# Optimization experiments

Measured on AMD Instinct MI355X. Metric: run time of the kernel, lower is better.

## Reference

```python
import jax, jax.numpy as jnp
import numpy as np

D_HEAD = 64
IGNORE = -100000.0


def setup_inputs() -> dict:
    key = jax.random.key(0)
    ks = jax.random.split(key, 5)
    B, S, D, H, M = 2, 2048, 768, 12, D_HEAD
    scale = 0.05  # 'random_normal' keras init stddev
    return {
        "x": jax.random.normal(ks[0], (B, S, D), jnp.float32),
        "W_Q": jax.random.normal(ks[1], (H, D, M), jnp.float32) * scale,
        "b_Q": jnp.zeros((H, M), jnp.float32),
        "W_K": jax.random.normal(ks[2], (H, D, M), jnp.float32) * scale,
        "b_K": jnp.zeros((H, M), jnp.float32),
        "W_V": jax.random.normal(ks[3], (H, D, M), jnp.float32) * scale,
        "b_V": jnp.zeros((H, M), jnp.float32),
        "W_O": jax.random.normal(ks[4], (H, M, D), jnp.float32) * scale,
        "b_O": jnp.zeros((D,), jnp.float32),
    }


def reference(x, W_Q, b_Q, W_K, b_K, W_V, b_V, W_O, b_O):
    # q,k,v: [b, s, h, m]
    q = jnp.einsum("bqd,hdm->bqhm", x, W_Q) + b_Q
    k = jnp.einsum("bkd,hdm->bkhm", x, W_K) + b_K
    v = jnp.einsum("bkd,hdm->bkhm", x, W_V) + b_V
    # scores: [b, h, q, k], scaled by 1/sqrt(d_head)
    scores = jnp.einsum("bqhm,bkhm->bhqk", q, k) / jnp.sqrt(
        jnp.asarray(D_HEAD, q.dtype)
    )
    S = x.shape[1]
    # causal mask: strictly-upper-triangular positions set to IGNORE (-1e5),
    # matching tf.where(mask == 1, IGNORE, scores)
    causal = jnp.arange(S)[:, None] >= jnp.arange(S)[None, :]  # [q, k]
    scores = jnp.where(causal[None, None, :, :], scores, jnp.asarray(IGNORE, scores.dtype))
    pattern = jax.nn.softmax(scores, axis=-1)
    z = jnp.einsum("bhqk,bkhm->bqhm", pattern, v)
    attn_out = jnp.einsum("bqhm,hmd->bqd", z, W_O) + b_O
    return attn_out
```

## Files before the change

### kernel.cpp

```cpp
#include <hip/hip_runtime.h>
#include <hip/hip_bf16.h>
#include <cstdint>
#include <cstddef>

#define B_ 2
#define S_ 2048
#define D_ 768
#define H_ 12
#define M_ 64
#define BS_ (B_ * S_)
#define NQKV_ 2304
#define NCHUNK_ 80
#define TOTCHUNK_ (24 * NCHUNK_)
#define QSCALE 0.18033688011f

typedef __attribute__((ext_vector_type(8))) short bf16x8;
typedef __attribute__((ext_vector_type(4))) short bf16x4;
typedef __attribute__((ext_vector_type(4))) float f32x4;

__device__ __forceinline__ unsigned short f2bu(float f) {
    __hip_bfloat16 h = __float2bfloat16(f);
    unsigned short u;
    __builtin_memcpy(&u, &h, 2);
    return u;
}
__device__ __forceinline__ unsigned pack2(float a, float b) {
    return (unsigned)f2bu(a) | ((unsigned)f2bu(b) << 16);
}

__device__ __forceinline__ bf16x8 ld16(const unsigned short* p) {
    p = (const unsigned short*)__builtin_assume_aligned(p, 16);
    bf16x8 v; __builtin_memcpy(&v, p, 16); return v;
}
__device__ __forceinline__ bf16x4 ld8(const unsigned short* p) {
    p = (const unsigned short*)__builtin_assume_aligned(p, 8);
    bf16x4 v; __builtin_memcpy(&v, p, 8); return v;
}
__device__ __forceinline__ uint4 ld16u(const unsigned short* p) {
    p = (const unsigned short*)__builtin_assume_aligned(p, 16);
    uint4 v; __builtin_memcpy(&v, p, 16); return v;
}
__device__ __forceinline__ void st16(unsigned short* p, uint4 v) {
    p = (unsigned short*)__builtin_assume_aligned(p, 16);
    __builtin_memcpy(p, &v, 16);
}
__device__ __forceinline__ void st8(unsigned short* p, uint2 v) {
    p = (unsigned short*)__builtin_assume_aligned(p, 8);
    __builtin_memcpy(p, &v, 8);
}
__device__ __forceinline__ float4 ldf4(const float* p) {
    p = (const float*)__builtin_assume_aligned(p, 16);
    float4 v; __builtin_memcpy(&v, p, 16); return v;
}
__device__ __forceinline__ void async16(const unsigned short* g, unsigned short* l) {
    __builtin_amdgcn_global_load_lds(
        (const __attribute__((address_space(1))) void*)g,
        (__attribute__((address_space(3))) void*)l, 16, 0, 0);
}
__device__ __forceinline__ void b82f(uint4 u, float* o) {
    o[0] = __uint_as_float(u.x << 16); o[1] = __uint_as_float(u.x & 0xffff0000u);
    o[2] = __uint_as_float(u.y << 16); o[3] = __uint_as_float(u.y & 0xffff0000u);
    o[4] = __uint_as_float(u.z << 16); o[5] = __uint_as_float(u.z & 0xffff0000u);
    o[6] = __uint_as_float(u.w << 16); o[7] = __uint_as_float(u.w & 0xffff0000u);
}

#define NEG_BIG (-3.0e38f)

__global__ void prep(const float* __restrict__ WQ, const float* __restrict__ WK,
                     const float* __restrict__ WV, const float* __restrict__ WO,
                     const float* __restrict__ x,
                     unsigned short* __restrict__ WT,
                     unsigned short* __restrict__ WOT,
                     unsigned short* __restrict__ xb)
{
    const int bx = blockIdx.x;
    if (bx < 216) {
        const int xx = bx % 9, yy = bx / 9;
        const int c  = xx * 256 + threadIdx.x;
        const int k0 = yy * 32;
        const int which = c / D_;
        const int r = c - which * D_;
        const int h = r >> 6, m = r & 63;
        const float* Wsel = (which == 0) ? WQ : (which == 1) ? WK : WV;
        const float* src = Wsel + (size_t)h * D_ * M_ + m;
        unsigned short* dst = WT + (size_t)c * D_ + k0;
        for (int i = 0; i < 32; i += 8) {
            float wv[8];
#pragma unroll
            for (int j = 0; j < 8; j++) wv[j] = src[(size_t)(k0 + i + j) * M_];
            uint4 pu;
            pu.x = pack2(wv[0], wv[1]); pu.y = pack2(wv[2], wv[3]);
            pu.z = pack2(wv[4], wv[5]); pu.w = pack2(wv[6], wv[7]);
            st16(dst + i, pu);
        }
    } else if (bx < 288) {
        const int b2 = bx - 216;
        const int xx = b2 % 3, yy = b2 / 3;
        const int c  = xx * 256 + threadIdx.x;
        const int k0 = yy * 32;
        unsigned short* dst = WOT + (size_t)c * D_ + k0;
        for (int i = 0; i < 32; i += 8) {
            float wv[8];
#pragma unroll
            for (int j = 0; j < 8; j++) wv[j] = WO[(size_t)(k0 + i + j) * D_ + c];
            uint4 pu;
            pu.x = pack2(wv[0], wv[1]); pu.y = pack2(wv[2], wv[3]);
            pu.z = pack2(wv[4], wv[5]); pu.w = pack2(wv[6], wv[7]);
            st16(dst + i, pu);
        }
    } else {
        const size_t i = ((size_t)(bx - 288) * 256 + threadIdx.x) * 16;
#pragma unroll
        for (int p = 0; p < 2; p++) {
            float4 a0 = ldf4(x + i + p * 8), a1 = ldf4(x + i + p * 8 + 4);
            uint4 u;
            u.x = pack2(a0.x, a0.y); u.y = pack2(a0.z, a0.w);
            u.z = pack2(a1.x, a1.y); u.w = pack2(a1.z, a1.w);
            st16(xb + i + p * 8, u);
        }
    }
}

__global__ __launch_bounds__(256, 2) void qkv_gemm(
    const unsigned short* __restrict__ xb,
    const unsigned short* __restrict__ WT,
    const float* __restrict__ bQ, const float* __restrict__ bK,
    const float* __restrict__ bV,
    unsigned short* __restrict__ qo, unsigned short* __restrict__ ko,
    unsigned short* __restrict__ vt)
{
    const int row0 = blockIdx.x * 128;
    const int col0 = blockIdx.y * 96;
    const int t = threadIdx.x;
    const int w = t >> 6, lane = t & 63, quad = lane >> 4, l16 = lane & 15;
    const int wrow0 = (w & 1) * 64, wcol0 = (w >> 1) * 48;

    __shared__ unsigned short Alds[128 * 64];
    __shared__ unsigned short Blds[96 * 64];

    f32x4 acc[4][3] = {};

    const unsigned short* asrc[4];
    const unsigned short* bsrc[3];
    int ldsoffA[4], ldsoffB[3];
#pragma unroll
    for (int q = 0; q < 4; q++) {
        const int cq = w * 256 + q * 64 + lane;
        const int row = cq >> 3, c = cq & 7;
        const int cs = c ^ (row & 7);
        asrc[q] = xb + (size_t)(row0 + row) * D_ + cs * 8;
        ldsoffA[q] = (w * 256 + q * 64) * 8;
    }
#pragma unroll
    for (int q = 0; q < 3; q++) {
        const int cq = w * 192 + q * 64 + lane;
        const int row = cq >> 3, c = cq & 7;
        const int cs = c ^ (row & 7);
        bsrc[q] = WT + (size_t)(col0 + row) * D_ + cs * 8;
        ldsoffB[q] = (w * 192 + q * 64) * 8;
    }
    const int swz = (l16 & 7);

    for (int k0 = 0; k0 < D_; k0 += 64) {
#pragma unroll
        for (int q = 0; q < 4; q++) async16(asrc[q] + k0, Alds + ldsoffA[q]);
#pragma unroll
        for (int q = 0; q < 3; q++) async16(bsrc[q] + k0, Blds + ldsoffB[q]);
        __syncthreads();

        bf16x8 af[4][2], bfm[3][2];
#pragma unroll
        for (int rt = 0; rt < 4; rt++) {
            const int row = wrow0 + rt * 16 + l16;
#pragma unroll
            for (int hh = 0; hh < 2; hh++)
                af[rt][hh] = ld16(&Alds[row * 64 + ((hh * 4 + quad) ^ swz) * 8]);
        }
#pragma unroll
        for (int st = 0; st < 3; st++) {
            const int row = wcol0 + st * 16 + l16;
#pragma unroll
            for (int hh = 0; hh < 2; hh++)
                bfm[st][hh] = ld16(&Blds[row * 64 + ((hh * 4 + quad) ^ swz) * 8]);
        }
#pragma unroll
        for (int rt = 0; rt < 4; rt++)
#pragma unroll
            for (int st = 0; st < 3; st++) {
                acc[rt][st] = __builtin_amdgcn_mfma_f32_16x16x32_bf16(
                    af[rt][0], bfm[st][0], acc[rt][st], 0, 0, 0);
                acc[rt][st] = __builtin_amdgcn_mfma_f32_16x16x32_bf16(
                    af[rt][1], bfm[st][1], acc[rt][st], 0, 0, 0);
            }
        __syncthreads();
    }

    const int which = col0 / D_;
    const int colin = col0 - which * D_;

    if (which == 0) {
#pragma unroll
        for (int st = 0; st < 3; st++) {
            const int cl = colin + wcol0 + st * 16 + l16;
            const int h = cl >> 6, m = cl & 63;
            const float bval = bQ[cl];
#pragma unroll
            for (int rt = 0; rt < 4; rt++)
#pragma unroll
                for (int rr = 0; rr < 4; rr++) {
                    const int R = row0 + wrow0 + rt * 16 + quad * 4 + rr;
                    const int bb = R >> 11, s = R & (S_ - 1);
                    qo[(((size_t)bb * H_ + h) * S_ + s) * M_ + m] =
                        f2bu((acc[rt][st][rr] + bval) * QSCALE);
                }
        }
    } else if (which == 1) {
#pragma unroll
        for (int st = 0; st < 3; st++) {
            const int cl = colin + wcol0 + st * 16 + l16;
            const int h = cl >> 6, m = cl & 63;
            const int blk = m >> 3, inn = m & 7;
            const float bval = bK[cl];
#pragma unroll
            for (int rt = 0; rt < 4; rt++)
#pragma unroll
                for (int rr = 0; rr < 4; rr++) {
                    const int R = row0 + wrow0 + rt * 16 + quad * 4 + rr;
                    const int bb = R >> 11, s = R & (S_ - 1);
                    ko[(((size_t)bb * H_ + h) * S_ + s) * M_ +
                       ((blk ^ (s & 7)) << 3) + inn] =
                        f2bu(acc[rt][st][rr] + bval);
                }
        }
    } else {
#pragma unroll
        for (int st = 0; st < 3; st++) {
            const int cl = colin + wcol0 + st * 16 + l16;
            const int h = cl >> 6, m = cl & 63;
            const float bval = bV[cl];
#pragma unroll
            for (int rt = 0; rt < 4; rt++) {
                const int R0 = row0 + wrow0 + rt * 16 + quad * 4;
                const int bb = R0 >> 11, s0 = R0 & (S_ - 1);
                const int tile = s0 >> 7;
                const int gl = (s0 & 127) >> 2;
                const int pl = gl >> 1, hi = gl & 1;
                const int pp = pl ^ ((m >> 1) & 7);
                const int half = hi ^ (m & 1);
                uint2 v;
                v.x = pack2(acc[rt][st][0] + bval, acc[rt][st][1] + bval);
                v.y = pack2(acc[rt][st][2] + bval, acc[rt][st][3] + bval);
                st8(&vt[(((size_t)bb * H_ + h) * 16 + tile) * (M_ * 128)
                        + m * 128 + (pp * 2 + half) * 4], v);
            }
        }
    }
}

__global__ __launch_bounds__(256, 2) void attn_split(
    const unsigned short* __restrict__ Q,
    const unsigned short* __restrict__ Kin,
    const unsigned short* __restrict__ Vt,
    unsigned short* __restrict__ Opart,
    float* __restrict__ ml,
    unsigned short* __restrict__ Z)
{
    const int flat = blockIdx.y * NCHUNK_ + blockIdx.x;
    const int bh = flat % 24;
    const int xx = (NCHUNK_ - 1) - flat / 24;

    int qt, c, nc;
    if (xx < 8)       { qt = xx; c = 0; nc = 1; }
    else if (xx < 24) { int u = xx - 8;  qt = 8  + (u >> 1); c = u & 1;  nc = 2; }
    else if (xx < 48) { int u = xx - 24; qt = 16 + u / 3;    c = u % 3;  nc = 3; }
    else              { int u = xx - 48; qt = 24 + (u >> 2); c = u & 3;  nc = 4; }

    const int ci     = bh * NCHUNK_ + xx;
    const int kbeg   = c * 512;
    const int keyend = min((qt + 1) * 64, kbeg + 512);
    const int iters  = (keyend - kbeg + 127) >> 7;
    const bool lastchunk = (c == nc - 1);

    const int t = threadIdx.x;
    const int wave = t >> 6, lane = t & 63, quad = lane >> 4, l16 = lane & 15;

    const unsigned short* Qb  = Q   + ((size_t)bh * S_ + qt * 64) * M_;
    const unsigned short* Kb  = Kin + (size_t)bh * S_ * M_;
    const unsigned short* Vb  = Vt  + (size_t)bh * M_ * S_;

    __shared__ unsigned short Klds[128 * 64];
    __shared__ unsigned short Vlds[64 * 128];

    bf16x8 qf[2];
    {
        const unsigned short* qrow = Qb + (size_t)(wave * 16 + l16) * M_;
        qf[0] = ld16(qrow + quad * 8);
        qf[1] = ld16(qrow + 32 + quad * 8);
    }

    const int ksw = l16 & 7;
    const int ko0 = (quad ^ ksw) * 8;
    const int ko1 = ((quad + 4) ^ ksw) * 8;
    int voff[8];
#pragma unroll
    for (int st = 0; st < 8; st++)
        voff[st] = l16 * 128 + (quad ^ (l16 & 3)) * 4
                 + ((st ^ ((l16 >> 2) & 3)) << 4);

    const int wdst = wave * 64 * 8;

    f32x4 o_acc[4] = {};
    float lrow = 0.f;

    for (int it = 0; it < iters; it++) {
        __syncthreads();
        const int key0 = kbeg + it * 128;
        const unsigned short* kt = Kb + (size_t)key0 * M_;
        const unsigned short* vtile = Vb + (size_t)(key0 >> 7) * (M_ * 128);
#pragma unroll
        for (int q = 0; q < 4; q++)
            async16(kt + (size_t)(q * 256 + t) * 8, Klds + q * 2048 + wdst);
#pragma unroll
        for (int q = 0; q < 4; q++)
            async16(vtile + (size_t)(q * 256 + t) * 8, Vlds + q * 2048 + wdst);
        __syncthreads();

        f32x4 s_acc[8];
#pragma unroll
        for (int st = 0; st < 8; st++) {
            f32x4 z4 = {0.f, 0.f, 0.f, 0.f};
            const unsigned short* krow = &Klds[(st * 16 + l16) * 64];
            bf16x8 k0 = ld16(krow + ko0);
            bf16x8 k1 = ld16(krow + ko1);
            z4 = __builtin_amdgcn_mfma_f32_16x16x32_bf16(k0, qf[0], z4, 0, 0, 0);
            z4 = __builtin_amdgcn_mfma_f32_16x16x32_bf16(k1, qf[1], z4, 0, 0, 0);
            s_acc[st] = z4;
        }

        if (lastchunk && it == iters - 1) {
            const int keyq = kbeg + it * 128 + quad * 4;
            const int qg = qt * 64 + wave * 16 + l16;
#pragma unroll
            for (int st = 0; st < 8; st++)
#pragma unroll
                for (int r = 0; r < 4; r++)
                    if (keyq + st * 16 + r > qg)
                        s_acc[st][r] = -1e30f;
        }

        bf16x4 pkv[8];
#pragma unroll
        for (int st = 0; st < 8; st++) {
            float p0 = exp2f(s_acc[st][0]);
            float p1 = exp2f(s_acc[st][1]);
            float p2 = exp2f(s_acc[st][2]);
            float p3 = exp2f(s_acc[st][3]);
            lrow += (p0 + p1) + (p2 + p3);
            uint2 u;
            u.x = pack2(p0, p1);
            u.y = pack2(p2, p3);
            __builtin_memcpy(&pkv[st], &u, 8);
        }

#pragma unroll
        for (int stf = 0; stf < 4; stf++) {
#pragma unroll
            for (int st = 0; st < 8; st++) {
                bf16x4 va = ld8(&Vlds[stf * 2048 + voff[st]]);
                o_acc[stf] = __builtin_amdgcn_mfma_f32_16x16x16bf16_1k(
                    va, pkv[st], o_acc[stf], 0, 0, 0);
            }
        }
    }

    lrow += __shfl_xor(lrow, 16, 64);
    lrow += __shfl_xor(lrow, 32, 64);

    const int q = wave * 16 + l16;
    if (nc == 1) {
        const float invL = 1.0f / lrow;
        const int b = bh / H_, h = bh - b * H_;
        unsigned short* zp =
            Z + ((size_t)b * S_ + qt * 64 + q) * (H_ * M_) + h * M_;
#pragma unroll
        for (int stf = 0; stf < 4; stf++) {
            uint2 u;
            u.x = pack2(o_acc[stf][0] * invL, o_acc[stf][1] * invL);
            u.y = pack2(o_acc[stf][2] * invL, o_acc[stf][3] * invL);
            st8(&zp[stf * 16 + quad * 4], u);
        }
    } else {
        unsigned short* Op = Opart + (size_t)ci * 4096;
#pragma unroll
        for (int stf = 0; stf < 4; stf++) {
            uint2 u;
            u.x = pack2(o_acc[stf][0], o_acc[stf][1]);
            u.y = pack2(o_acc[stf][2], o_acc[stf][3]);
            st8(&Op[q * 64 + stf * 16 + quad * 4], u);
        }
        if (quad == 0)
            ml[(size_t)ci * 128 + 64 + q] = lrow;
    }
}

__global__ void combine(const unsigned short* __restrict__ Opart,
                        const float* __restrict__ ml,
                        unsigned short* __restrict__ Z)
{
    const int qt = blockIdx.x + 8, bh = blockIdx.y;
    const int b = bh / H_, h = bh - b * H_;
    const int g = qt >> 3, r7 = qt & 7;
    const int nc = g + 1;
    const int base = bh * NCHUNK_ + qt + 4 * g * (g - 1) + r7 * g;

    const int t = threadIdx.x;
    const int q = t >> 2, fs = (t & 3) * 16;

    float L = 0.f;
    for (int c = 0; c < nc; c++)
        L += ml[(size_t)(base + c) * 128 + 64 + q];
    const float invL = 1.0f / L;

    float o[16] = {};
    for (int c = 0; c < nc; c++) {
        const unsigned short* op =
            Opart + (size_t)(base + c) * 4096 + q * 64 + fs;
        float f[8];
        b82f(ld16u(op), f);
#pragma unroll
        for (int j = 0; j < 8; j++) o[j] += f[j];
        b82f(ld16u(op + 8), f);
#pragma unroll
        for (int j = 0; j < 8; j++) o[8 + j] += f[j];
    }

    unsigned short* zp =
        Z + ((size_t)b * S_ + qt * 64 + q) * (H_ * M_) + h * M_ + fs;
    uint4 u0, u1;
    u0.x = pack2(o[0]*invL,  o[1]*invL);  u0.y = pack2(o[2]*invL,  o[3]*invL);
    u0.z = pack2(o[4]*invL,  o[5]*invL);  u0.w = pack2(o[6]*invL,  o[7]*invL);
    u1.x = pack2(o[8]*invL,  o[9]*invL);  u1.y = pack2(o[10]*invL, o[11]*invL);
    u1.z = pack2(o[12]*invL, o[13]*invL); u1.w = pack2(o[14]*invL, o[15]*invL);
    st16(zp, u0);
    st16(zp + 8, u1);
}

__global__ __launch_bounds__(256, 2) void oproj_gemm(
    const unsigned short* __restrict__ Zin,
    const unsigned short* __restrict__ WOT,
    const float* __restrict__ bO,
    float* __restrict__ out)
{
    const int row0 = blockIdx.x * 64;
    const int col0 = blockIdx.y * 128;
    const int t = threadIdx.x;
    const int w = t >> 6, lane = t & 63, quad = lane >> 4, l16 = lane & 15;
    const int wrow0 = (w & 1) * 32, wcol0 = (w >> 1) * 64;

    __shared__ unsigned short Alds[64 * 64];
    __shared__ unsigned short Blds[128 * 64];

    f32x4 acc[2][4] = {};

    const unsigned short* asrc[2];
    const unsigned short* bsrc[4];
    int ldsoffA[2], ldsoffB[4];
#pragma unroll
    for (int q = 0; q < 2; q++) {
        const int cq = w * 128 + q * 64 + lane;
        const int row = cq >> 3, c = cq & 7;
        const int cs = c ^ (row & 7);
        asrc[q] = Zin + (size_t)(row0 + row) * D_ + cs * 8;
        ldsoffA[q] = (w * 128 + q * 64) * 8;
    }
#pragma unroll
    for (int q = 0; q < 4; q++) {
        const int cq = w * 256 + q * 64 + lane;
        const int row = cq >> 3, c = cq & 7;
        const int cs = c ^ (row & 7);
        bsrc[q] = WOT + (size_t)(col0 + row) * D_ + cs * 8;
        ldsoffB[q] = (w * 256 + q * 64) * 8;
    }
    const int swz = (l16 & 7);

    for (int k0 = 0; k0 < D_; k0 += 64) {
#pragma unroll
        for (int q = 0; q < 2; q++) async16(asrc[q] + k0, Alds + ldsoffA[q]);
#pragma unroll
        for (int q = 0; q < 4; q++) async16(bsrc[q] + k0, Blds + ldsoffB[q]);
        __syncthreads();

        bf16x8 af[2][2], bfm[4][2];
#pragma unroll
        for (int rt = 0; rt < 2; rt++) {
            const int row = wrow0 + rt * 16 + l16;
#pragma unroll
            for (int hh = 0; hh < 2; hh++)
                af[rt][hh] = ld16(&Alds[row * 64 + ((hh * 4 + quad) ^ swz) * 8]);
        }
#pragma unroll
        for (int st = 0; st < 4; st++) {
            const int row = wcol0 + st * 16 + l16;
#pragma unroll
            for (int hh = 0; hh < 2; hh++)
                bfm[st][hh] = ld16(&Blds[row * 64 + ((hh * 4 + quad) ^ swz) * 8]);
        }
#pragma unroll
        for (int rt = 0; rt < 2; rt++)
#pragma unroll
            for (int st = 0; st < 4; st++) {
                acc[rt][st] = __builtin_amdgcn_mfma_f32_16x16x32_bf16(
                    af[rt][0], bfm[st][0], acc[rt][st], 0, 0, 0);
                acc[rt][st] = __builtin_amdgcn_mfma_f32_16x16x32_bf16(
                    af[rt][1], bfm[st][1], acc[rt][st], 0, 0, 0);
            }
        __syncthreads();
    }

#pragma unroll
    for (int st = 0; st < 4; st++) {
        const int c = col0 + wcol0 + st * 16 + l16;
        const float bval = bO[c];
#pragma unroll
        for (int rt = 0; rt < 2; rt++)
#pragma unroll
            for (int rr = 0; rr < 4; rr++) {
                const int R = row0 + wrow0 + rt * 16 + quad * 4 + rr;
                out[(size_t)R * D_ + c] = acc[rt][st][rr] + bval;
            }
    }
}

extern "C" void kernel_launch(void* const* d_in, const int* in_sizes, int n_in,
                              void* d_out, int out_size, void* d_ws, size_t ws_size,
                              hipStream_t stream)
{
    const float* x  = (const float*)d_in[0];
    const float* WQ = (const float*)d_in[1];
    const float* bQ = (const float*)d_in[2];
    const float* WK = (const float*)d_in[3];
    const float* bK = (const float*)d_in[4];
    const float* WV = (const float*)d_in[5];
    const float* bV = (const float*)d_in[6];
    const float* WO = (const float*)d_in[7];
    const float* bO = (const float*)d_in[8];
    float* out = (float*)d_out;

    const size_t n = (size_t)B_ * H_ * S_ * M_;
    unsigned short* q_ws  = (unsigned short*)d_ws;
    unsigned short* k_ws  = q_ws + n;
    unsigned short* vt_ws = k_ws + n;
    unsigned short* z_ws  = vt_ws + n;
    unsigned short* WT    = z_ws + n;
    unsigned short* WOT   = WT + (size_t)NQKV_ * D_;
    unsigned short* xb    = WOT + (size_t)D_ * D_;
    unsigned short* Opart = xb + (size_t)BS_ * D_;
    float* mlbuf = (float*)(Opart + (size_t)TOTCHUNK_ * 4096);

    prep<<<dim3(1056), 256, 0, stream>>>(WQ, WK, WV, WO, x, WT, WOT, xb);
    qkv_gemm<<<dim3(BS_ / 128, NQKV_ / 96), 256, 0, stream>>>(
        xb, WT, bQ, bK, bV, q_ws, k_ws, vt_ws);
    attn_split<<<dim3(NCHUNK_, B_ * H_), 256, 0, stream>>>(
        q_ws, k_ws, vt_ws, Opart, mlbuf, z_ws);
    combine<<<dim3(S_ / 64 - 8, B_ * H_), 256, 0, stream>>>(
        Opart, mlbuf, z_ws);
    oproj_gemm<<<dim3(BS_ / 64, D_ / 128), 256, 0, stream>>>(
        z_ws, WOT, bO, out);
}
```

Baseline: 150.2 us.

## Process 128 query rows per attention block to reuse K/V tiles twice

Each attention block now handles two 64-row query sub-tiles against every K/V tile loaded into shared memory. This halves the number of chunks and the global-to-LDS K/V traffic per query. The chunk indexing, partial-output buffers and the combine kernel are adjusted to match. In exchange each block holds twice the accumulators, which raises register pressure, and there are fewer blocks to spread across the GPU.

```diff
diff --git a/kernel.cpp b/kernel.cpp
--- a/kernel.cpp
+++ b/kernel.cpp
@@ -10,7 +10,7 @@
 #define M_ 64
 #define BS_ (B_ * S_)
 #define NQKV_ 2304
-#define NCHUNK_ 80
+#define NCHUNK_ 40
 #define TOTCHUNK_ (24 * NCHUNK_)
 #define QSCALE 0.18033688011f
 
@@ -269,33 +269,36 @@
     const int bh = flat % 24;
     const int xx = (NCHUNK_ - 1) - flat / 24;
 
-    int qt, c, nc;
-    if (xx < 8)       { qt = xx; c = 0; nc = 1; }
-    else if (xx < 24) { int u = xx - 8;  qt = 8  + (u >> 1); c = u & 1;  nc = 2; }
-    else if (xx < 48) { int u = xx - 24; qt = 16 + u / 3;    c = u % 3;  nc = 3; }
-    else              { int u = xx - 48; qt = 24 + (u >> 2); c = u & 3;  nc = 4; }
-
-    const int ci     = bh * NCHUNK_ + xx;
+    int qt2, c, nc;
+    if (xx < 4)       { qt2 = xx; c = 0; nc = 1; }
+    else if (xx < 12) { int u = xx - 4;  qt2 = 4  + (u >> 1); c = u & 1; nc = 2; }
+    else if (xx < 24) { int u = xx - 12; qt2 = 8  + u / 3;    c = u % 3; nc = 3; }
+    else              { int u = xx - 24; qt2 = 12 + (u >> 2); c = u & 3; nc = 4; }
+
+    const int g = qt2 >> 2, r4 = qt2 & 3;
+    const int ci = bh * NCHUNK_ + qt2 + 2 * g * (g - 1) + r4 * g + c;
     const int kbeg   = c * 512;
-    const int keyend = min((qt + 1) * 64, kbeg + 512);
-    const int iters  = (keyend - kbeg + 127) >> 7;
+    const int keyend = min((qt2 + 1) * 128, kbeg + 512);
+    const int iters  = (keyend - kbeg) >> 7;
     const bool lastchunk = (c == nc - 1);
 
     const int t = threadIdx.x;
     const int wave = t >> 6, lane = t & 63, quad = lane >> 4, l16 = lane & 15;
 
-    const unsigned short* Qb  = Q   + ((size_t)bh * S_ + qt * 64) * M_;
+    const unsigned short* Qb  = Q   + ((size_t)bh * S_ + qt2 * 128) * M_;
     const unsigned short* Kb  = Kin + (size_t)bh * S_ * M_;
     const unsigned short* Vb  = Vt  + (size_t)bh * M_ * S_;
 
     __shared__ unsigned short Klds[128 * 64];
     __shared__ unsigned short Vlds[64 * 128];
 
-    bf16x8 qf[2];
-    {
-        const unsigned short* qrow = Qb + (size_t)(wave * 16 + l16) * M_;
-        qf[0] = ld16(qrow + quad * 8);
-        qf[1] = ld16(qrow + 32 + quad * 8);
+    bf16x8 qf[2][2];
+#pragma unroll
+    for (int sub = 0; sub < 2; sub++) {
+        const unsigned short* qrow =
+            Qb + (size_t)(sub * 64 + wave * 16 + l16) * M_;
+        qf[sub][0] = ld16(qrow + quad * 8);
+        qf[sub][1] = ld16(qrow + 32 + quad * 8);
     }
 
     const int ksw = l16 & 7;
@@ -309,8 +312,8 @@
 
     const int wdst = wave * 64 * 8;
 
-    f32x4 o_acc[4] = {};
-    float lrow = 0.f;
+    f32x4 o_acc[2][4] = {};
+    float lrow[2] = {0.f, 0.f};
 
     for (int it = 0; it < iters; it++) {
         __syncthreads();
@@ -325,81 +328,97 @@
             async16(vtile + (size_t)(q * 256 + t) * 8, Vlds + q * 2048 + wdst);
         __syncthreads();
 
-        f32x4 s_acc[8];
-#pragma unroll
-        for (int st = 0; st < 8; st++) {
-            f32x4 z4 = {0.f, 0.f, 0.f, 0.f};
-            const unsigned short* krow = &Klds[(st * 16 + l16) * 64];
-            bf16x8 k0 = ld16(krow + ko0);
-            bf16x8 k1 = ld16(krow + ko1);
-            z4 = __builtin_amdgcn_mfma_f32_16x16x32_bf16(k0, qf[0], z4, 0, 0, 0);
-            z4 = __builtin_amdgcn_mfma_f32_16x16x32_bf16(k1, qf[1], z4, 0, 0, 0);
-            s_acc[st] = z4;
-        }
-
-        if (lastchunk && it == iters - 1) {
-            const int keyq = kbeg + it * 128 + quad * 4;
-            const int qg = qt * 64 + wave * 16 + l16;
-#pragma unroll
-            for (int st = 0; st < 8; st++)
-#pragma unroll
-                for (int r = 0; r < 4; r++)
-                    if (keyq + st * 16 + r > qg)
-                        s_acc[st][r] = -1e30f;
-        }
-
-        bf16x4 pkv[8];
-#pragma unroll
-        for (int st = 0; st < 8; st++) {
-            float p0 = exp2f(s_acc[st][0]);
-            float p1 = exp2f(s_acc[st][1]);
-            float p2 = exp2f(s_acc[st][2]);
-            float p3 = exp2f(s_acc[st][3]);
-            lrow += (p0 + p1) + (p2 + p3);
-            uint2 u;
-            u.x = pack2(p0, p1);
-            u.y = pack2(p2, p3);
-            __builtin_memcpy(&pkv[st], &u, 8);
-        }
-
-#pragma unroll
-        for (int stf = 0; stf < 4; stf++) {
+        const bool maskit = lastchunk && (it == iters - 1);
+
+#pragma unroll
+        for (int sub = 0; sub < 2; sub++) {
+            f32x4 s_acc[8];
 #pragma unroll
             for (int st = 0; st < 8; st++) {
-                bf16x4 va = ld8(&Vlds[stf * 2048 + voff[st]]);
-                o_acc[stf] = __builtin_amdgcn_mfma_f32_16x16x16bf16_1k(
-                    va, pkv[st], o_acc[stf], 0, 0, 0);
-            }
-        }
-    }
-
-    lrow += __shfl_xor(lrow, 16, 64);
-    lrow += __shfl_xor(lrow, 32, 64);
-
-    const int q = wave * 16 + l16;
+                f32x4 z4 = {0.f, 0.f, 0.f, 0.f};
+                const unsigned short* krow = &Klds[(st * 16 + l16) * 64];
+                bf16x8 k0 = ld16(krow + ko0);
+                bf16x8 k1 = ld16(krow + ko1);
+                z4 = __builtin_amdgcn_mfma_f32_16x16x32_bf16(k0, qf[sub][0], z4, 0, 0, 0);
+                z4 = __builtin_amdgcn_mfma_f32_16x16x32_bf16(k1, qf[sub][1], z4, 0, 0, 0);
+                s_acc[st] = z4;
+            }
+
+            if (maskit) {
+                const int keyq = kbeg + it * 128 + quad * 4;
+                const int qg = qt2 * 128 + sub * 64 + wave * 16 + l16;
+#pragma unroll
+                for (int st = 0; st < 8; st++)
+#pragma unroll
+                    for (int r = 0; r < 4; r++)
+                        if (keyq + st * 16 + r > qg)
+                            s_acc[st][r] = -1e30f;
+            }
+
+            bf16x4 pkv[8];
+#pragma unroll
+            for (int st = 0; st < 8; st++) {
+                float p0 = exp2f(s_acc[st][0]);
+                float p1 = exp2f(s_acc[st][1]);
+                float p2 = exp2f(s_acc[st][2]);
+                float p3 = exp2f(s_acc[st][3]);
+                lrow[sub] += (p0 + p1) + (p2 + p3);
+                uint2 u;
+                u.x = pack2(p0, p1);
+                u.y = pack2(p2, p3);
+                __builtin_memcpy(&pkv[st], &u, 8);
+            }
+
+#pragma unroll
+            for (int stf = 0; stf < 4; stf++) {
+#pragma unroll
+                for (int st = 0; st < 8; st++) {
+                    bf16x4 va = ld8(&Vlds[stf * 2048 + voff[st]]);
+                    o_acc[sub][stf] = __builtin_amdgcn_mfma_f32_16x16x16bf16_1k(
+                        va, pkv[st], o_acc[sub][stf], 0, 0, 0);
+                }
+            }
+        }
+    }
+
+#pragma unroll
+    for (int sub = 0; sub < 2; sub++) {
+        lrow[sub] += __shfl_xor(lrow[sub], 16, 64);
+        lrow[sub] += __shfl_xor(lrow[sub], 32, 64);
+    }
+
+    const int qb = wave * 16 + l16;
     if (nc == 1) {
-        const float invL = 1.0f / lrow;
         const int b = bh / H_, h = bh - b * H_;
-        unsigned short* zp =
-            Z + ((size_t)b * S_ + qt * 64 + q) * (H_ * M_) + h * M_;
-#pragma unroll
-        for (int stf = 0; stf < 4; stf++) {
-            uint2 u;
-            u.x = pack2(o_acc[stf][0] * invL, o_acc[stf][1] * invL);
-            u.y = pack2(o_acc[stf][2] * invL, o_acc[stf][3] * invL);
-            st8(&zp[stf * 16 + quad * 4], u);
+#pragma unroll
+        for (int sub = 0; sub < 2; sub++) {
+            const float invL = 1.0f / lrow[sub];
+            unsigned short* zp =
+                Z + ((size_t)b * S_ + qt2 * 128 + sub * 64 + qb) * (H_ * M_)
+                  + h * M_;
+#pragma unroll
+            for (int stf = 0; stf < 4; stf++) {
+                uint2 u;
+                u.x = pack2(o_acc[sub][stf][0] * invL, o_acc[sub][stf][1] * invL);
+                u.y = pack2(o_acc[sub][stf][2] * invL, o_acc[sub][stf][3] * invL);
+                st8(&zp[stf * 16 + quad * 4], u);
+            }
         }
     } else {
-        unsigned short* Op = Opart + (size_t)ci * 4096;
-#pragma unroll
-        for (int stf = 0; stf < 4; stf++) {
-            uint2 u;
-            u.x = pack2(o_acc[stf][0], o_acc[stf][1]);
-            u.y = pack2(o_acc[stf][2], o_acc[stf][3]);
-            st8(&Op[q * 64 + stf * 16 + quad * 4], u);
-        }
-        if (quad == 0)
-            ml[(size_t)ci * 128 + 64 + q] = lrow;
+        unsigned short* Op = Opart + (size_t)ci * 8192;
+#pragma unroll
+        for (int sub = 0; sub < 2; sub++) {
+            const int q = sub * 64 + qb;
+#pragma unroll
+            for (int stf = 0; stf < 4; stf++) {
+                uint2 u;
+                u.x = pack2(o_acc[sub][stf][0], o_acc[sub][stf][1]);
+                u.y = pack2(o_acc[sub][stf][2], o_acc[sub][stf][3]);
+                st8(&Op[q * 64 + stf * 16 + quad * 4], u);
+            }
+            if (quad == 0)
+                ml[(size_t)ci * 128 + q] = lrow[sub];
+        }
     }
 }
 
@@ -407,24 +426,24 @@
                         const float* __restrict__ ml,
                         unsigned short* __restrict__ Z)
 {
-    const int qt = blockIdx.x + 8, bh = blockIdx.y;
+    const int qt2 = blockIdx.x + 4, bh = blockIdx.y;
     const int b = bh / H_, h = bh - b * H_;
-    const int g = qt >> 3, r7 = qt & 7;
+    const int g = qt2 >> 2, r4 = qt2 & 3;
     const int nc = g + 1;
-    const int base = bh * NCHUNK_ + qt + 4 * g * (g - 1) + r7 * g;
+    const int base = bh * NCHUNK_ + qt2 + 2 * g * (g - 1) + r4 * g;
 
     const int t = threadIdx.x;
     const int q = t >> 2, fs = (t & 3) * 16;
 
     float L = 0.f;
     for (int c = 0; c < nc; c++)
-        L += ml[(size_t)(base + c) * 128 + 64 + q];
+        L += ml[(size_t)(base + c) * 128 + q];
     const float invL = 1.0f / L;
 
     float o[16] = {};
     for (int c = 0; c < nc; c++) {
         const unsigned short* op =
-            Opart + (size_t)(base + c) * 4096 + q * 64 + fs;
+            Opart + (size_t)(base + c) * 8192 + q * 64 + fs;
         float f[8];
         b82f(ld16u(op), f);
 #pragma unroll
@@ -435,7 +454,7 @@
     }
 
     unsigned short* zp =
-        Z + ((size_t)b * S_ + qt * 64 + q) * (H_ * M_) + h * M_ + fs;
+        Z + ((size_t)b * S_ + qt2 * 128 + q) * (H_ * M_) + h * M_ + fs;
     uint4 u0, u1;
     u0.x = pack2(o[0]*invL,  o[1]*invL);  u0.y = pack2(o[2]*invL,  o[3]*invL);
     u0.z = pack2(o[4]*invL,  o[5]*invL);  u0.w = pack2(o[6]*invL,  o[7]*invL);
@@ -555,14 +574,14 @@
     unsigned short* WOT   = WT + (size_t)NQKV_ * D_;
     unsigned short* xb    = WOT + (size_t)D_ * D_;
     unsigned short* Opart = xb + (size_t)BS_ * D_;
-    float* mlbuf = (float*)(Opart + (size_t)TOTCHUNK_ * 4096);
+    float* mlbuf = (float*)(Opart + (size_t)TOTCHUNK_ * 8192);
 
     prep<<<dim3(1056), 256, 0, stream>>>(WQ, WK, WV, WO, x, WT, WOT, xb);
     qkv_gemm<<<dim3(BS_ / 128, NQKV_ / 96), 256, 0, stream>>>(
         xb, WT, bQ, bK, bV, q_ws, k_ws, vt_ws);
     attn_split<<<dim3(NCHUNK_, B_ * H_), 256, 0, stream>>>(
         q_ws, k_ws, vt_ws, Opart, mlbuf, z_ws);
-    combine<<<dim3(S_ / 64 - 8, B_ * H_), 256, 0, stream>>>(
+    combine<<<dim3(12, B_ * H_), 512, 0, stream>>>(
         Opart, mlbuf, z_ws);
     oproj_gemm<<<dim3(BS_ / 64, D_ / 128), 256, 0, stream>>>(
         z_ws, WOT, bO, out);
```

Result: slower. 156.8 us (+4.4%).

## Use 128-query tiles with 512-thread blocks in split attention

Applied to the files above, without the earlier changes.

Each attention block now handles 128 query rows with 8 waves instead of 64 rows with 4 waves, so every K/V tile loaded into LDS is shared by twice as many queries. The chunk count per head drops from 80 to 40, and the chunk indexing, partial-output stride, ml layout and combine kernel are changed to match. This halves K/V global and LDS load traffic per query. The cost is fewer, larger blocks at one block per CU, which lowers occupancy and makes causal load balancing coarser.

```diff
diff --git a/kernel.cpp b/kernel.cpp
--- a/kernel.cpp
+++ b/kernel.cpp
@@ -10,7 +10,7 @@
 #define M_ 64
 #define BS_ (B_ * S_)
 #define NQKV_ 2304
-#define NCHUNK_ 80
+#define NCHUNK_ 40
 #define TOTCHUNK_ (24 * NCHUNK_)
 #define QSCALE 0.18033688011f
 
@@ -257,7 +257,7 @@
     }
 }
 
-__global__ __launch_bounds__(256, 2) void attn_split(
+__global__ __launch_bounds__(512, 1) void attn_split(
     const unsigned short* __restrict__ Q,
     const unsigned short* __restrict__ Kin,
     const unsigned short* __restrict__ Vt,
@@ -269,22 +269,23 @@
     const int bh = flat % 24;
     const int xx = (NCHUNK_ - 1) - flat / 24;
 
-    int qt, c, nc;
-    if (xx < 8)       { qt = xx; c = 0; nc = 1; }
-    else if (xx < 24) { int u = xx - 8;  qt = 8  + (u >> 1); c = u & 1;  nc = 2; }
-    else if (xx < 48) { int u = xx - 24; qt = 16 + u / 3;    c = u % 3;  nc = 3; }
-    else              { int u = xx - 48; qt = 24 + (u >> 2); c = u & 3;  nc = 4; }
-
-    const int ci     = bh * NCHUNK_ + xx;
+    int qt2, c, nc;
+    if (xx < 4)       { qt2 = xx; c = 0; nc = 1; }
+    else if (xx < 12) { int u = xx - 4;  qt2 = 4  + (u >> 1); c = u & 1; nc = 2; }
+    else if (xx < 24) { int u = xx - 12; qt2 = 8  + u / 3;    c = u % 3; nc = 3; }
+    else              { int u = xx - 24; qt2 = 12 + (u >> 2); c = u & 3; nc = 4; }
+
+    const int g = qt2 >> 2, r4 = qt2 & 3;
+    const int ci = bh * NCHUNK_ + qt2 + 2 * g * (g - 1) + r4 * g + c;
     const int kbeg   = c * 512;
-    const int keyend = min((qt + 1) * 64, kbeg + 512);
-    const int iters  = (keyend - kbeg + 127) >> 7;
+    const int keyend = min((qt2 + 1) * 128, kbeg + 512);
+    const int iters  = (keyend - kbeg) >> 7;
     const bool lastchunk = (c == nc - 1);
 
     const int t = threadIdx.x;
     const int wave = t >> 6, lane = t & 63, quad = lane >> 4, l16 = lane & 15;
 
-    const unsigned short* Qb  = Q   + ((size_t)bh * S_ + qt * 64) * M_;
+    const unsigned short* Qb  = Q   + ((size_t)bh * S_ + qt2 * 128) * M_;
     const unsigned short* Kb  = Kin + (size_t)bh * S_ * M_;
     const unsigned short* Vb  = Vt  + (size_t)bh * M_ * S_;
 
@@ -318,11 +319,11 @@
         const unsigned short* kt = Kb + (size_t)key0 * M_;
         const unsigned short* vtile = Vb + (size_t)(key0 >> 7) * (M_ * 128);
 #pragma unroll
-        for (int q = 0; q < 4; q++)
-            async16(kt + (size_t)(q * 256 + t) * 8, Klds + q * 2048 + wdst);
-#pragma unroll
-        for (int q = 0; q < 4; q++)
-            async16(vtile + (size_t)(q * 256 + t) * 8, Vlds + q * 2048 + wdst);
+        for (int q = 0; q < 2; q++)
+            async16(kt + (size_t)(q * 512 + t) * 8, Klds + q * 4096 + wdst);
+#pragma unroll
+        for (int q = 0; q < 2; q++)
+            async16(vtile + (size_t)(q * 512 + t) * 8, Vlds + q * 4096 + wdst);
         __syncthreads();
 
         f32x4 s_acc[8];
@@ -339,7 +340,7 @@
 
         if (lastchunk && it == iters - 1) {
             const int keyq = kbeg + it * 128 + quad * 4;
-            const int qg = qt * 64 + wave * 16 + l16;
+            const int qg = qt2 * 128 + wave * 16 + l16;
 #pragma unroll
             for (int st = 0; st < 8; st++)
 #pragma unroll
@@ -381,7 +382,7 @@
         const float invL = 1.0f / lrow;
         const int b = bh / H_, h = bh - b * H_;
         unsigned short* zp =
-            Z + ((size_t)b * S_ + qt * 64 + q) * (H_ * M_) + h * M_;
+            Z + ((size_t)b * S_ + qt2 * 128 + q) * (H_ * M_) + h * M_;
 #pragma unroll
         for (int stf = 0; stf < 4; stf++) {
             uint2 u;
@@ -390,7 +391,7 @@
             st8(&zp[stf * 16 + quad * 4], u);
         }
     } else {
-        unsigned short* Op = Opart + (size_t)ci * 4096;
+        unsigned short* Op = Opart + (size_t)ci * 8192;
 #pragma unroll
         for (int stf = 0; stf < 4; stf++) {
             uint2 u;
@@ -399,7 +400,7 @@
             st8(&Op[q * 64 + stf * 16 + quad * 4], u);
         }
         if (quad == 0)
-            ml[(size_t)ci * 128 + 64 + q] = lrow;
+            ml[(size_t)ci * 128 + q] = lrow;
     }
 }
 
@@ -407,24 +408,24 @@
                         const float* __restrict__ ml,
                         unsigned short* __restrict__ Z)
 {
-    const int qt = blockIdx.x + 8, bh = blockIdx.y;
+    const int qt2 = blockIdx.x + 4, bh = blockIdx.y;
     const int b = bh / H_, h = bh - b * H_;
-    const int g = qt >> 3, r7 = qt & 7;
+    const int g = qt2 >> 2, r4 = qt2 & 3;
     const int nc = g + 1;
-    const int base = bh * NCHUNK_ + qt + 4 * g * (g - 1) + r7 * g;
+    const int base = bh * NCHUNK_ + qt2 + 2 * g * (g - 1) + r4 * g;
 
     const int t = threadIdx.x;
     const int q = t >> 2, fs = (t & 3) * 16;
 
     float L = 0.f;
     for (int c = 0; c < nc; c++)
-        L += ml[(size_t)(base + c) * 128 + 64 + q];
+        L += ml[(size_t)(base + c) * 128 + q];
     const float invL = 1.0f / L;
 
     float o[16] = {};
     for (int c = 0; c < nc; c++) {
         const unsigned short* op =
-            Opart + (size_t)(base + c) * 4096 + q * 64 + fs;
+            Opart + (size_t)(base + c) * 8192 + q * 64 + fs;
         float f[8];
         b82f(ld16u(op), f);
 #pragma unroll
@@ -435,7 +436,7 @@
     }
 
     unsigned short* zp =
-        Z + ((size_t)b * S_ + qt * 64 + q) * (H_ * M_) + h * M_ + fs;
+        Z + ((size_t)b * S_ + qt2 * 128 + q) * (H_ * M_) + h * M_ + fs;
     uint4 u0, u1;
     u0.x = pack2(o[0]*invL,  o[1]*invL);  u0.y = pack2(o[2]*invL,  o[3]*invL);
     u0.z = pack2(o[4]*invL,  o[5]*invL);  u0.w = pack2(o[6]*invL,  o[7]*invL);
@@ -555,14 +556,14 @@
     unsigned short* WOT   = WT + (size_t)NQKV_ * D_;
     unsigned short* xb    = WOT + (size_t)D_ * D_;
     unsigned short* Opart = xb + (size_t)BS_ * D_;
-    float* mlbuf = (float*)(Opart + (size_t)TOTCHUNK_ * 4096);
+    float* mlbuf = (float*)(Opart + (size_t)TOTCHUNK_ * 8192);
 
     prep<<<dim3(1056), 256, 0, stream>>>(WQ, WK, WV, WO, x, WT, WOT, xb);
     qkv_gemm<<<dim3(BS_ / 128, NQKV_ / 96), 256, 0, stream>>>(
         xb, WT, bQ, bK, bV, q_ws, k_ws, vt_ws);
-    attn_split<<<dim3(NCHUNK_, B_ * H_), 256, 0, stream>>>(
+    attn_split<<<dim3(NCHUNK_, B_ * H_), 512, 0, stream>>>(
         q_ws, k_ws, vt_ws, Opart, mlbuf, z_ws);
-    combine<<<dim3(S_ / 64 - 8, B_ * H_), 256, 0, stream>>>(
+    combine<<<dim3(12, B_ * H_), 512, 0, stream>>>(
         Opart, mlbuf, z_ws);
     oproj_gemm<<<dim3(BS_ / 64, D_ / 128), 256, 0, stream>>>(
         z_ws, WOT, bO, out);
```

Measured after the change: 161.5 us. 1.08x slower.
